# Kernel optimization log

Hardware: AMD Instinct MI355X
Metric: run time of the kernel (lower is better)

Reference implementation:

```python
import jax, jax.numpy as jnp
import numpy as np

N_STEPS = 128
N_UNITS = 2048
BATCH = 256
DT = 1e-3
TAU_M = 10.0 * DT            # NeuroTorch LIFLayer default tau_m
ALPHA = float(np.exp(-DT / TAU_M))  # membrane decay factor
THRESHOLD = 1.0
GAMMA = 100.0                # surrogate-gradient sharpness


@jax.custom_vjp
def heaviside_spike(v):
    # forward: hard threshold; backward: sigmoid surrogate (see fwdbwd module)
    return (v > THRESHOLD).astype(v.dtype)

def _hs_fwd(v):
    return heaviside_spike(v), v

def _hs_bwd(v, g):
    sig = jax.nn.sigmoid(GAMMA * (v - THRESHOLD))
    return (g * GAMMA * sig * (1.0 - sig),)

heaviside_spike.defvjp(_hs_fwd, _hs_bwd)


def setup_inputs() -> dict:
    key = jax.random.key(0)
    kx, kw = jax.random.split(key)
    x = jax.random.normal(kx, (BATCH, N_UNITS), dtype=jnp.float32)
    # LIF feedforward weights (n_units -> n_units), no recurrent connection
    W = (jax.random.normal(kw, (N_UNITS, N_UNITS), dtype=jnp.float32)
         / np.float32(np.sqrt(N_UNITS)))
    return {"x": x, "W": W}


def reference(x, W):
    # x: (B, N) analog input; first "spike" frame is the raw input (as in source).
    def step(carry, _):
        x_fwd, V, Z = carry
        I = x_fwd @ W                                   # (B, N)
        # reset term uses detached spikes in the original (stop_gradient)
        V_next = ALPHA * V * (1.0 - jax.lax.stop_gradient(Z)) + I
        Z_next = heaviside_spike(V_next)
        return (Z_next, V_next, Z_next), Z_next

    V0 = jnp.zeros_like(x)
    Z0 = jnp.zeros_like(x)
    _, spikes = jax.lax.scan(step, (x, V0, Z0), None, length=N_STEPS - 1)
    # spikes: (n_steps-1, B, N); prepend the analog frame -> stack along time
    out = jnp.concatenate([x[None], spikes], axis=0)    # (T, B, N)
    return jnp.transpose(out, (1, 0, 2))                # (B, T, N)
```

## Files before the change

kernel.cpp:

```cpp
#include <hip/hip_runtime.h>
#include <stdint.h>


#define BATCHSZ 256
#define NU      2048
#define TSTEPS  128
#define BLK     1024
#define NWAVES  (BLK / 64)

#define D_BN 128
#define D_BM 8

__global__ __launch_bounds__(128) void lif_dense_v1(
    const float* __restrict__ x,
    const float* __restrict__ W,
    float* __restrict__ ws)
{
    __shared__ float s_x[D_BM * NU];

    const int tid  = threadIdx.x;
    const int lane = tid & 63;

    const int bid    = blockIdx.x;
    const int xcd    = bid & 7;
    const int w      = bid >> 3;
    const int n_tile = xcd * 2 + (w >> 5);
    const int m_tile = w & 31;
    const int n0     = n_tile * D_BN;
    const int m0     = m_tile * D_BM;

    {
        const float4* xg = (const float4*)(x + (size_t)m0 * NU);
        float4*       xs = (float4*)s_x;
        #pragma unroll
        for (int j = 0; j < 32; ++j)
            xs[j * 128 + tid] = xg[j * 128 + tid];
    }
    __syncthreads();

    const int rb = (tid >> 6) * 4;
    const float* xw = &s_x[rb * NU];
    const float* wp = W + n0 + lane * 2;

    float2 wA[16], wB[16];
    float4 xA[16], xB[16];
    float2 acc[4];
    #pragma unroll
    for (int r = 0; r < 4; ++r) { acc[r].x = 0.0f; acc[r].y = 0.0f; }

    #pragma unroll
    for (int j = 0; j < 16; ++j)
        wA[j] = *(const float2*)(wp + (size_t)j * NU);
    #pragma unroll
    for (int q = 0; q < 4; ++q)
        #pragma unroll
        for (int r = 0; r < 4; ++r)
            xA[q * 4 + r] = *(const float4*)&xw[r * NU + q * 4];

    for (int k0 = 0; k0 < NU; k0 += 32) {
        #pragma unroll
        for (int j = 0; j < 16; ++j)
            wB[j] = *(const float2*)(wp + (size_t)(k0 + 16 + j) * NU);
        #pragma unroll
        for (int q = 0; q < 4; ++q)
            #pragma unroll
            for (int r = 0; r < 4; ++r)
                xB[q * 4 + r] = *(const float4*)&xw[r * NU + k0 + 16 + q * 4];

        #pragma unroll
        for (int q = 0; q < 4; ++q)
            #pragma unroll
            for (int kk = 0; kk < 4; ++kk) {
                float2 wv = wA[q * 4 + kk];
                #pragma unroll
                for (int r = 0; r < 4; ++r) {
                    float xv = ((const float*)&xA[q * 4 + r])[kk];
                    acc[r].x = __builtin_fmaf(xv, wv.x, acc[r].x);
                    acc[r].y = __builtin_fmaf(xv, wv.y, acc[r].y);
                }
            }

        if (k0 + 32 < NU) {
            #pragma unroll
            for (int j = 0; j < 16; ++j)
                wA[j] = *(const float2*)(wp + (size_t)(k0 + 32 + j) * NU);
            #pragma unroll
            for (int q = 0; q < 4; ++q)
                #pragma unroll
                for (int r = 0; r < 4; ++r)
                    xA[q * 4 + r] = *(const float4*)&xw[r * NU + k0 + 32 + q * 4];
        }

        #pragma unroll
        for (int q = 0; q < 4; ++q)
            #pragma unroll
            for (int kk = 0; kk < 4; ++kk) {
                float2 wv = wB[q * 4 + kk];
                #pragma unroll
                for (int r = 0; r < 4; ++r) {
                    float xv = ((const float*)&xB[q * 4 + r])[kk];
                    acc[r].x = __builtin_fmaf(xv, wv.x, acc[r].x);
                    acc[r].y = __builtin_fmaf(xv, wv.y, acc[r].y);
                }
            }
    }

    #pragma unroll
    for (int r = 0; r < 4; ++r)
        *(float2*)&ws[(size_t)(m0 + rb + r) * NU + n0 + lane * 2] = acc[r];
}

__global__ __launch_bounds__(BLK) void lif_recurrence(
    const float* __restrict__ x,
    const float* __restrict__ W,
    const float* __restrict__ V1,
    float* __restrict__ out)
{
    const int b    = blockIdx.x;
    const int tid  = threadIdx.x;
    const int lane = tid & 63;
    const int wid  = tid >> 6;

    __shared__ int           s_idx[NU];
    __shared__ unsigned char s_flag[NU];
    __shared__ int           s_wsum[NWAVES];
    __shared__ int           s_cnt;

    const int n0 = tid;
    const int n1 = tid + BLK;

    float* outb = out + (size_t)b * TSTEPS * NU;

    float V0, V1r;
    int   z0, z1;
    {
        float x0 = x[(size_t)b * NU + n0];
        float x1 = x[(size_t)b * NU + n1];
        outb[n0] = x0;
        outb[n1] = x1;
        V0  = V1[(size_t)b * NU + n0];
        V1r = V1[(size_t)b * NU + n1];
        z0 = V0  > 1.0f;
        z1 = V1r > 1.0f;
        float* f1 = outb + NU;
        f1[n0] = z0 ? 1.0f : 0.0f;
        f1[n1] = z1 ? 1.0f : 0.0f;
        s_flag[n0] = (unsigned char)z0;
        s_flag[n1] = (unsigned char)z1;
    }
    __syncthreads();

    for (int t = 2; t < TSTEPS; ++t) {
        int f0 = s_flag[2 * tid];
        int f1 = s_flag[2 * tid + 1];
        int c  = f0 + f1;
        int v  = c;
        #pragma unroll
        for (int d = 1; d < 64; d <<= 1) {
            int o = __shfl_up(v, d);
            if (lane >= d) v += o;
        }
        if (lane == 63) s_wsum[wid] = v;
        __syncthreads();
        int base = 0;
        #pragma unroll
        for (int w = 0; w < NWAVES; ++w) base += (w < wid) ? s_wsum[w] : 0;
        int off = base + v - c;
        if (f0) s_idx[off++] = (2 * tid) * NU;
        if (f1) s_idx[off]   = (2 * tid + 1) * NU;
        if (tid == BLK - 1) s_cnt = base + v;
        __syncthreads();

        int cnt = s_cnt;
        if (cnt == 0) {
            size_t  elems  = (size_t)(TSTEPS - t) * NU;
            float4* p      = (float4*)(outb + (size_t)t * NU);
            int     chunks = (int)(elems / 4);
            float4  zz; zz.x = zz.y = zz.z = zz.w = 0.0f;
            for (int i = tid; i < chunks; i += BLK) p[i] = zz;
            return;
        }

        float I0 = 0.0f, I1 = 0.0f;
        const float* Wc = W + tid;
        int i = 0;
        for (; i + 4 <= cnt; i += 4) {
            const float* r0 = Wc + s_idx[i];
            const float* r1 = Wc + s_idx[i + 1];
            const float* r2 = Wc + s_idx[i + 2];
            const float* r3 = Wc + s_idx[i + 3];
            float a0 = r0[0], b0 = r0[BLK];
            float a1 = r1[0], b1 = r1[BLK];
            float a2 = r2[0], b2 = r2[BLK];
            float a3 = r3[0], b3 = r3[BLK];
            I0 += a0; I0 += a1; I0 += a2; I0 += a3;
            I1 += b0; I1 += b1; I1 += b2; I1 += b3;
        }
        for (; i < cnt; ++i) {
            const float* r = Wc + s_idx[i];
            I0 += r[0];
            I1 += r[BLK];
        }

        float d0 = 0.90483741803595952f * V0;
        float d1 = 0.90483741803595952f * V1r;
        asm volatile("" : "+v"(d0), "+v"(d1));
        float nv0 = (z0 ? 0.0f : d0) + I0;
        float nv1 = (z1 ? 0.0f : d1) + I1;
        V0 = nv0; V1r = nv1;
        z0 = nv0 > 1.0f;
        z1 = nv1 > 1.0f;

        float* po = outb + (size_t)t * NU;
        po[n0] = z0 ? 1.0f : 0.0f;
        po[n1] = z1 ? 1.0f : 0.0f;
        s_flag[n0] = (unsigned char)z0;
        s_flag[n1] = (unsigned char)z1;
        __syncthreads();
    }
}

__global__ __launch_bounds__(BLK) void lif_fused(
    const float* __restrict__ x,
    const float* __restrict__ W,
    float* __restrict__ out)
{
    const int b    = blockIdx.x;
    const int tid  = threadIdx.x;
    const int lane = tid & 63;
    const int wid  = tid >> 6;

    __shared__ float         s_x[NU];
    __shared__ int           s_idx[NU];
    __shared__ unsigned char s_flag[NU];
    __shared__ int           s_wsum[NWAVES];
    __shared__ int           s_cnt;

    const int n0 = tid;
    const int n1 = tid + BLK;
    float* outb = out + (size_t)b * TSTEPS * NU;

    {
        float x0 = x[(size_t)b * NU + n0];
        float x1 = x[(size_t)b * NU + n1];
        s_x[n0] = x0; s_x[n1] = x1;
        outb[n0] = x0; outb[n1] = x1;
    }
    __syncthreads();

    float I0 = 0.0f, I1 = 0.0f;
    {
        const float* Wc = W + tid;
        #pragma unroll 8
        for (int k = 0; k < NU; ++k) {
            float xk = s_x[k];
            const float* wr = Wc + (size_t)k * NU;
            I0 = __builtin_fmaf(xk, wr[0],   I0);
            I1 = __builtin_fmaf(xk, wr[BLK], I1);
        }
    }

    float V0 = 0.0f, V1 = 0.0f;
    int   z0 = 0,    z1 = 0;

    for (int t = 1; t < TSTEPS; ++t) {
        if (t >= 2) {
            int f0 = s_flag[2 * tid];
            int f1 = s_flag[2 * tid + 1];
            int c  = f0 + f1;
            int v  = c;
            #pragma unroll
            for (int d = 1; d < 64; d <<= 1) {
                int o = __shfl_up(v, d);
                if (lane >= d) v += o;
            }
            if (lane == 63) s_wsum[wid] = v;
            __syncthreads();
            int base = 0;
            #pragma unroll
            for (int w = 0; w < NWAVES; ++w) base += (w < wid) ? s_wsum[w] : 0;
            int off = base + v - c;
            if (f0) s_idx[off++] = 2 * tid;
            if (f1) s_idx[off]   = 2 * tid + 1;
            if (tid == BLK - 1) s_cnt = base + v;
            __syncthreads();

            int cnt = s_cnt;
            if (cnt == 0) {
                size_t  elems  = (size_t)(TSTEPS - t) * NU;
                float4* p      = (float4*)(outb + (size_t)t * NU);
                int     chunks = (int)(elems / 4);
                float4  zz; zz.x = zz.y = zz.z = zz.w = 0.0f;
                for (int i = tid; i < chunks; i += BLK) p[i] = zz;
                return;
            }

            I0 = 0.0f; I1 = 0.0f;
            const float* Wc = W + tid;
            int i = 0;
            for (; i + 2 <= cnt; i += 2) {
                const float* r0 = Wc + (size_t)s_idx[i]     * NU;
                const float* r1 = Wc + (size_t)s_idx[i + 1] * NU;
                float a0 = r0[0], b0 = r0[BLK];
                float a1 = r1[0], b1 = r1[BLK];
                I0 += a0; I0 += a1;
                I1 += b0; I1 += b1;
            }
            for (; i < cnt; ++i) {
                const float* r = Wc + (size_t)s_idx[i] * NU;
                I0 += r[0];
                I1 += r[BLK];
            }
        }

        float d0 = 0.90483741803595952f * V0;
        float d1 = 0.90483741803595952f * V1;
        asm volatile("" : "+v"(d0), "+v"(d1));
        float nv0 = (z0 ? 0.0f : d0) + I0;
        float nv1 = (z1 ? 0.0f : d1) + I1;
        V0 = nv0; V1 = nv1;
        z0 = nv0 > 1.0f;
        z1 = nv1 > 1.0f;

        float* po = outb + (size_t)t * NU;
        po[n0] = z0 ? 1.0f : 0.0f;
        po[n1] = z1 ? 1.0f : 0.0f;
        s_flag[n0] = (unsigned char)z0;
        s_flag[n1] = (unsigned char)z1;
        __syncthreads();
    }
}

extern "C" void kernel_launch(void* const* d_in, const int* in_sizes, int n_in,
                              void* d_out, int out_size, void* d_ws, size_t ws_size,
                              hipStream_t stream) {
    const float* x = (const float*)d_in[0];
    const float* W = (const float*)d_in[1];
    if (n_in >= 2 && in_sizes[0] == NU * NU && in_sizes[1] == BATCHSZ * NU) {
        const float* t = x; x = W; W = t;
    }
    float* out = (float*)d_out;

    const size_t need = (size_t)BATCHSZ * NU * sizeof(float);
    if (ws_size >= need) {
        float* V1 = (float*)d_ws;
        hipLaunchKernelGGL(lif_dense_v1,
                           dim3(512), dim3(128), 0, stream,
                           x, W, V1);
        hipLaunchKernelGGL(lif_recurrence,
                           dim3(BATCHSZ), dim3(BLK), 0, stream,
                           x, W, V1, out);
    } else {
        hipLaunchKernelGGL(lif_fused, dim3(BATCHSZ), dim3(BLK), 0, stream,
                           x, W, out);
    }
}
```

Baseline: 168.4 us.

## Fuse output zero-fill into dense GEMM launch and drop LDS staging of x

Adds a second set of blocks to the dense GEMM kernel that bulk-zero most of the output tensor, so the recurrence kernel simply returns once no neurons spike instead of writing zeros itself. This moves the large zero-write traffic so it can overlap with the GEMM compute. The GEMM also reads x directly from global memory rather than staging it through shared memory, and remaps tiles so n-tiles alternate across consecutive blocks. Risks: the fill covers a fixed flat range that may not line up with the per-batch layout the recurrence writes, the same rows can be written twice, and uncached global reads of x may be slower than the shared-memory copy.

```diff
diff --git a/kernel.cpp b/kernel.cpp
--- a/kernel.cpp
+++ b/kernel.cpp
@@ -7,39 +7,43 @@
 #define TSTEPS  128
 #define BLK     1024
 #define NWAVES  (BLK / 64)
+#define BN_FR   (BATCHSZ * NU)
 
 #define D_BN 128
 #define D_BM 8
-
-__global__ __launch_bounds__(128) void lif_dense_v1(
+#define D_DENSE_BLOCKS 512
+#define D_FILL_BLOCKS  512
+
+__global__ __launch_bounds__(128) void lif_dense_fill(
     const float* __restrict__ x,
     const float* __restrict__ W,
-    float* __restrict__ ws)
+    float* __restrict__ ws,
+    float* __restrict__ out)
 {
-    __shared__ float s_x[D_BM * NU];
-
-    const int tid  = threadIdx.x;
+    const int bid = blockIdx.x;
+    const int tid = threadIdx.x;
+
+    if (bid >= D_DENSE_BLOCKS) {
+        const int    fid    = bid - D_DENSE_BLOCKS;
+        float4*      dst    = (float4*)(out + (size_t)2 * BN_FR);
+        const int    total  = (TSTEPS - 2) * BN_FR / 4;
+        const int    stride = D_FILL_BLOCKS * 128;
+        float4 zz; zz.x = zz.y = zz.z = zz.w = 0.0f;
+        for (int i = fid * 128 + tid; i < total; i += stride)
+            dst[i] = zz;
+        return;
+    }
+
     const int lane = tid & 63;
-
-    const int bid    = blockIdx.x;
     const int xcd    = bid & 7;
     const int w      = bid >> 3;
-    const int n_tile = xcd * 2 + (w >> 5);
-    const int m_tile = w & 31;
+    const int n_tile = xcd * 2 + (w & 1);
+    const int m_tile = w >> 1;
     const int n0     = n_tile * D_BN;
     const int m0     = m_tile * D_BM;
 
-    {
-        const float4* xg = (const float4*)(x + (size_t)m0 * NU);
-        float4*       xs = (float4*)s_x;
-        #pragma unroll
-        for (int j = 0; j < 32; ++j)
-            xs[j * 128 + tid] = xg[j * 128 + tid];
-    }
-    __syncthreads();
-
     const int rb = (tid >> 6) * 4;
-    const float* xw = &s_x[rb * NU];
+    const float* xw = x + (size_t)(m0 + rb) * NU;
     const float* wp = W + n0 + lane * 2;
 
     float2 wA[16], wB[16];
@@ -55,7 +59,7 @@
     for (int q = 0; q < 4; ++q)
         #pragma unroll
         for (int r = 0; r < 4; ++r)
-            xA[q * 4 + r] = *(const float4*)&xw[r * NU + q * 4];
+            xA[q * 4 + r] = *(const float4*)(xw + (size_t)r * NU + q * 4);
 
     for (int k0 = 0; k0 < NU; k0 += 32) {
         #pragma unroll
@@ -65,7 +69,7 @@
         for (int q = 0; q < 4; ++q)
             #pragma unroll
             for (int r = 0; r < 4; ++r)
-                xB[q * 4 + r] = *(const float4*)&xw[r * NU + k0 + 16 + q * 4];
+                xB[q * 4 + r] = *(const float4*)(xw + (size_t)r * NU + k0 + 16 + q * 4);
 
         #pragma unroll
         for (int q = 0; q < 4; ++q)
@@ -88,7 +92,7 @@
             for (int q = 0; q < 4; ++q)
                 #pragma unroll
                 for (int r = 0; r < 4; ++r)
-                    xA[q * 4 + r] = *(const float4*)&xw[r * NU + k0 + 32 + q * 4];
+                    xA[q * 4 + r] = *(const float4*)(xw + (size_t)r * NU + k0 + 32 + q * 4);
         }
 
         #pragma unroll
@@ -172,14 +176,7 @@
         __syncthreads();
 
         int cnt = s_cnt;
-        if (cnt == 0) {
-            size_t  elems  = (size_t)(TSTEPS - t) * NU;
-            float4* p      = (float4*)(outb + (size_t)t * NU);
-            int     chunks = (int)(elems / 4);
-            float4  zz; zz.x = zz.y = zz.z = zz.w = 0.0f;
-            for (int i = tid; i < chunks; i += BLK) p[i] = zz;
-            return;
-        }
+        if (cnt == 0) return;
 
         float I0 = 0.0f, I1 = 0.0f;
         const float* Wc = W + tid;
@@ -344,9 +341,9 @@
     const size_t need = (size_t)BATCHSZ * NU * sizeof(float);
     if (ws_size >= need) {
         float* V1 = (float*)d_ws;
-        hipLaunchKernelGGL(lif_dense_v1,
-                           dim3(512), dim3(128), 0, stream,
-                           x, W, V1);
+        hipLaunchKernelGGL(lif_dense_fill,
+                           dim3(D_DENSE_BLOCKS + D_FILL_BLOCKS), dim3(128),
+                           0, stream, x, W, V1, out);
         hipLaunchKernelGGL(lif_recurrence,
                            dim3(BATCHSZ), dim3(BLK), 0, stream,
                            x, W, V1, out);
```

After: 206.8 us. 1.23x slower.
